# Kernel optimization log

Hardware: AMD Instinct MI355X
Metric: run time of the kernel (lower is better)

The kernel has to match this reference:

```python
import jax, jax.numpy as jnp
import numpy as np

N_STATE = 1024
N_HEAD = 16
LENGTHS = np.array([512, 576, 640, 704, 768, 832, 896, 1024], dtype=np.int32)
BATCH = len(LENGTHS)
MAX_SEQLEN = int(LENGTHS.max())
N_CTX = int(LENGTHS.sum())


def setup_inputs() -> dict:
    key = jax.random.key(0)
    ks = jax.random.split(key, 8)
    d = N_STATE
    cu = np.concatenate([[0], np.cumsum(LENGTHS)]).astype(np.int32)
    return {
        "x": jax.random.normal(ks[0], (N_CTX, d), dtype=jnp.float32),
        "Wq": jax.random.normal(ks[1], (d, d), dtype=jnp.float32) * 0.02,
        "bq": jnp.zeros((d,), dtype=jnp.float32),
        "Wk": jax.random.normal(ks[2], (d, d), dtype=jnp.float32) * 0.02,
        "Wv": jax.random.normal(ks[3], (d, d), dtype=jnp.float32) * 0.02,
        "bv": jnp.zeros((d,), dtype=jnp.float32),
        "Wo": jax.random.normal(ks[4], (d, d), dtype=jnp.float32) * 0.02,
        "bo": jnp.zeros((d,), dtype=jnp.float32),
        "cu_seqlens": jnp.asarray(cu),
    }


def reference(x, Wq, bq, Wk, Wv, bv, Wo, bo, cu_seqlens):
    n_ctx, d = x.shape
    H, hd = N_HEAD, d // N_HEAD
    scale = hd ** -0.5
    B, S = BATCH, MAX_SEQLEN  # static pad shape

    # QKV projections (torch Linear convention: y = x @ W.T + b; key has no bias)
    q = (x @ Wq.T + bq).reshape(n_ctx, H, hd)
    k = (x @ Wk.T).reshape(n_ctx, H, hd)
    v = (x @ Wv.T + bv).reshape(n_ctx, H, hd)

    seqlens = cu_seqlens[1:] - cu_seqlens[:-1]          # [B]
    tok = jnp.arange(n_ctx)
    seg = jnp.searchsorted(cu_seqlens[1:], tok, side="right")  # [n_ctx] batch id
    pos = tok - cu_seqlens[seg]                          # [n_ctx] position in seq

    # scatter packed tokens into zero-padded [B, S, H, hd]
    qp = jnp.zeros((B, S, H, hd), q.dtype).at[seg, pos].set(q)
    kp = jnp.zeros((B, S, H, hd), k.dtype).at[seg, pos].set(k)
    vp = jnp.zeros((B, S, H, hd), v.dtype).at[seg, pos].set(v)

    valid = jnp.arange(S)[None, :] < seqlens[:, None]    # [B, S] key mask

    scores = jnp.einsum("bihd,bjhd->bhij", qp, kp) * scale   # [B, H, S, S]
    neg = -jnp.finfo(scores.dtype).max
    scores = jnp.where(valid[:, None, None, :], scores, neg)
    weights = jax.nn.softmax(scores, axis=-1)
    ctx = jnp.einsum("bhij,bjhd->bihd", weights, vp)         # [B, S, H, hd]

    # gather back to packed [n_ctx, d]
    packed = ctx[seg, pos].reshape(n_ctx, d)
    return packed @ Wo.T + bo
```

## Files before the change

### kernel.cpp

```cpp
#include <hip/hip_runtime.h>
#include <hip/hip_fp16.h>
#include <stdint.h>

#define NCTX 5952
#define NHEAD 16
#define NABLK 372
#define NWBLK 256

typedef _Float16 f16x8 __attribute__((ext_vector_type(8)));
typedef _Float16 f16x4 __attribute__((ext_vector_type(4)));
typedef float    f32x4 __attribute__((ext_vector_type(4)));

typedef const __attribute__((address_space(1))) void* gp1;
typedef __attribute__((address_space(3))) void* lp3;

__device__ __forceinline__ f32x4 mfma16(f16x8 a, f16x8 b, f32x4 c) {
    return __builtin_amdgcn_mfma_f32_16x16x32_f16(a, b, c, 0, 0, 0);
}

#define SBAR() do { __builtin_amdgcn_sched_barrier(0); \
                    __builtin_amdgcn_s_barrier();      \
                    __builtin_amdgcn_sched_barrier(0); } while (0)

__device__ const int kQT[9]    = {0, 4, 9, 14, 20, 26, 33, 40, 48};
__device__ const int kBASE8[8] = {0, 512, 1088, 1728, 2432, 3200, 4032, 4928};
__device__ const int kLEN[8]   = {512, 576, 640, 704, 768, 832, 896, 1024};


__global__ __launch_bounds__(256) void presplit_all(
    const float* __restrict__ x,
    const float* __restrict__ Wq, const float* __restrict__ Wk,
    const float* __restrict__ Wv, const float* __restrict__ Wo,
    _Float16* __restrict__ Ah, _Float16* __restrict__ Wh)
{
    constexpr int NAG = NABLK * 32 * 64;
    const int idx = blockIdx.x * 256 + threadIdx.x;
    const float* src;
    _Float16* dst;
    if (idx < NAG) {
        int chunk = idx >> 6, within = idx & 63;
        int t = chunk & 31, b = chunk >> 5;
        int rb = within >> 2, go = within & 3;
        int r = b * 16 + rb;
        int g = go ^ ((r >> 1) & 3);
        src = x + (size_t)r * 1024 + t * 32 + g * 8;
        dst = Ah + (size_t)idx * 8;
    } else {
        int i2 = idx - NAG;
        int chunk = i2 >> 6, within = i2 & 63;
        int t = chunk & 31, b = chunk >> 5;
        int rb = within >> 2, go = within & 3;
        int n = b * 16 + rb;
        int g = go ^ ((n >> 1) & 3);
        const float* s = (n < 1024) ? Wq : (n < 2048) ? Wk : (n < 3072) ? Wv : Wo;
        src = s + (size_t)(n & 1023) * 1024 + t * 32 + g * 8;
        dst = Wh + (size_t)i2 * 8;
    }
    f32x4 v0 = *(const f32x4*)src;
    f32x4 v1 = *(const f32x4*)(src + 4);
    f16x8 hv;
    #pragma unroll
    for (int e = 0; e < 4; ++e) { hv[e] = (_Float16)v0[e]; hv[4 + e] = (_Float16)v1[e]; }
    *(f16x8*)dst = hv;
}

template <int MODE>
__global__ __launch_bounds__(512) void gemm1p(
    const _Float16* __restrict__ Ag, const _Float16* __restrict__ Wg,
    const float* __restrict__ bq, const float* __restrict__ bv, const float* __restrict__ bo,
    _Float16* __restrict__ qh, _Float16* __restrict__ kh, _Float16* __restrict__ vt,
    float* __restrict__ outp)
{
    constexpr int BN   = (MODE == 0) ? 384 : 128;
    constexpr int MI   = 6;
    constexpr int NF   = BN / 64;
    constexpr int SPH  = (MODE == 0) ? 5 : 3;
    constexpr int SPL  = (MODE == 0) ? 4 : 2;
    constexpr int ABYT = 12288;
    constexpr int BBYT = BN * 64;
    constexpr int BUF  = ABYT + BBYT;
    constexpr int T    = 32;
    constexpr int WB0  = (MODE == 0) ? 0 : 192;

    __shared__ __align__(16) char lds[3 * BUF];

    int bid = blockIdx.x;
    bid = (bid & 7) * 31 + (bid >> 3);
    const int mt = bid % 31, nt = bid / 31;
    const int m0 = mt * 192, n0 = nt * BN;
    const int tid = threadIdx.x;
    const int w = tid >> 6, l = tid & 63;
    const int ls = l >> 4, lq = l & 15;
    const int wm = w >> 2, wn = w & 3;

    const int myspw = (w < 4) ? SPH : SPL;
    const int fbase = (w < 4) ? w * SPH : 4 * SPH + (w - 4) * SPL;

    const char* sbase[5];
    int ldst[5];
    #pragma unroll
    for (int s = 0; s < 5; ++s) {
        if (s < myspw) {
            int f = fbase + s;
            if (f < 12) sbase[s] = (const char*)Ag + ((size_t)(m0 / 16 + f) * 32) * 1024;
            else        sbase[s] = (const char*)Wg + ((size_t)(WB0 + n0 / 16 + (f - 12)) * 32) * 1024;
            ldst[s] = f * 1024;
        } else { sbase[s] = nullptr; ldst[s] = 0; }
    }
    const int l16 = l * 16;
    auto STG = [&](int buf, int t2) {
        #pragma unroll
        for (int s = 0; s < 5; ++s)
            if (s < myspw)
                __builtin_amdgcn_global_load_lds((gp1)(sbase[s] + (size_t)t2 * 1024 + l16),
                                                 (lp3)(lds + buf * BUF + ldst[s]), 16, 0, 0);
    };

    int aoA[MI], aoB[NF];
    #pragma unroll
    for (int i = 0; i < MI; ++i) {
        int r = wm * 96 + i * 16 + lq;
        aoA[i] = r * 64 + 16 * (ls ^ ((r >> 1) & 3));
    }
    #pragma unroll
    for (int j = 0; j < NF; ++j) {
        int r = wn * (16 * NF) + j * 16 + lq;
        aoB[j] = ABYT + r * 64 + 16 * (ls ^ ((r >> 1) & 3));
    }

    f32x4 acc[MI][NF] = {};

    STG(0, 0);
    STG(1, 1);
    if (w < 4) { if constexpr (SPH == 5) asm volatile("s_waitcnt vmcnt(5)" ::: "memory");
                 else                    asm volatile("s_waitcnt vmcnt(3)" ::: "memory"); }
    else       { if constexpr (SPL == 4) asm volatile("s_waitcnt vmcnt(4)" ::: "memory");
                 else                    asm volatile("s_waitcnt vmcnt(2)" ::: "memory"); }
    SBAR();

    int cb = 0, pb = 2;
    #pragma unroll 1
    for (int t = 0; t < T; ++t) {
        const bool pf = (t + 2 < T);
        const char* cbp = lds + cb * BUF;
        if (pf) STG(pb, t + 2);

        f16x8 ah[MI], b[NF];
        #pragma unroll
        for (int i = 0; i < MI; ++i) ah[i] = *(const f16x8*)(cbp + aoA[i]);
        #pragma unroll
        for (int j = 0; j < NF; ++j) b[j] = *(const f16x8*)(cbp + aoB[j]);
        __builtin_amdgcn_s_setprio(1);
        #pragma unroll
        for (int i = 0; i < MI; ++i)
            #pragma unroll
            for (int j = 0; j < NF; ++j)
                acc[i][j] = mfma16(ah[i], b[j], acc[i][j]);
        __builtin_amdgcn_s_setprio(0);

        if (pf) {
            if (w < 4) { if constexpr (SPH == 5) asm volatile("s_waitcnt vmcnt(5) lgkmcnt(0)" ::: "memory");
                         else                    asm volatile("s_waitcnt vmcnt(3) lgkmcnt(0)" ::: "memory"); }
            else       { if constexpr (SPL == 4) asm volatile("s_waitcnt vmcnt(4) lgkmcnt(0)" ::: "memory");
                         else                    asm volatile("s_waitcnt vmcnt(2) lgkmcnt(0)" ::: "memory"); }
        } else {
            asm volatile("s_waitcnt vmcnt(0) lgkmcnt(0)" ::: "memory");
        }
        SBAR();
        cb = (cb == 2) ? 0 : cb + 1;
        pb = (pb == 2) ? 0 : pb + 1;
    }

    #pragma unroll
    for (int i = 0; i < MI; ++i)
        #pragma unroll
        for (int j = 0; j < NF; ++j) {
            const int mb = m0 + wm * 96 + i * 16 + 4 * ls;
            const int n  = n0 + wn * (16 * NF) + j * 16 + lq;
            if (MODE == 0) {
                const int which = n >> 10, nn = n & 1023;
                const int hh = nn >> 6, dd = nn & 63;
                if (which == 2) {
                    f16x4 vv;
                    #pragma unroll
                    for (int r = 0; r < 4; ++r) vv[r] = (_Float16)(acc[i][j][r] + bv[nn]);
                    *(f16x4*)&vt[((size_t)hh * 64 + dd) * NCTX + mb] = vv;
                } else if (which == 0) {
                    #pragma unroll
                    for (int r = 0; r < 4; ++r)
                        qh[((size_t)hh * NCTX + mb + r) * 64 + dd] = (_Float16)(acc[i][j][r] + bq[nn]);
                } else {
                    #pragma unroll
                    for (int r = 0; r < 4; ++r)
                        kh[((size_t)hh * NCTX + mb + r) * 64 + dd] = (_Float16)acc[i][j][r];
                }
            } else {
                #pragma unroll
                for (int r = 0; r < 4; ++r)
                    outp[(size_t)(mb + r) * 1024 + n] = acc[i][j][r] + bo[n];
            }
        }
}

__global__ __launch_bounds__(256) void attn_kernel(
    const _Float16* __restrict__ qh, const _Float16* __restrict__ kh,
    const _Float16* __restrict__ vt,
    _Float16* __restrict__ Ahc)
{
    __shared__ alignas(16) _Float16 KT[2][64][64];
    __shared__ alignas(16) _Float16 VT[2][64][64];
    __shared__ alignas(16) _Float16 P[4][2][16][64];
    const int bid = blockIdx.x;
    const int hd = bid & 15, t = bid >> 4;
    int b = 0;
    while (t >= kQT[b + 1]) ++b;
    const int kbase = kBASE8[b];
    const int L = kLEN[b];
    const int w = threadIdx.x >> 6, l = threadIdx.x & 63;
    const int ls = l >> 4, lq = l & 15;
    const int xm = lq & 7;
    const int q0l = (t - kQT[b]) * 128 + w * 32;
    const bool active = (q0l < L);
    const int q0 = kbase + q0l;

    const _Float16* kb = kh + (size_t)hd * NCTX * 64;
    const _Float16* vb = vt + (size_t)hd * 64 * NCTX;

    const char* ksrc[2]; const char* vsrc[2]; int sdst[2];
    #pragma unroll
    for (int s = 0; s < 2; ++s) {
        int G = w * 128 + s * 64 + l;
        int row = G >> 3, g = G & 7;
        ksrc[s] = (const char*)(kb + ((size_t)(kbase + row)) * 64 + (size_t)((g ^ (row & 7)) * 8));
        vsrc[s] = (const char*)(vb + (size_t)row * NCTX + kbase + (size_t)((g ^ (row & 7)) * 8));
        sdst[s] = (w * 128 + s * 64) * 16;
    }
    auto STG = [&](int buf, int t2) {
        #pragma unroll
        for (int s = 0; s < 2; ++s)
            __builtin_amdgcn_global_load_lds((gp1)(ksrc[s] + (size_t)t2 * 8192),
                                             (lp3)((char*)&KT[buf][0][0] + sdst[s]), 16, 0, 0);
        #pragma unroll
        for (int s = 0; s < 2; ++s)
            __builtin_amdgcn_global_load_lds((gp1)(vsrc[s] + (size_t)t2 * 128),
                                             (lp3)((char*)&VT[buf][0][0] + sdst[s]), 16, 0, 0);
    };

    f16x8 qf[2][2];
    if (active) {
        #pragma unroll
        for (int qg = 0; qg < 2; ++qg) {
            const _Float16* qp = qh + ((size_t)hd * NCTX + q0 + qg * 16 + lq) * 64 + ls * 8;
            qf[qg][0] = *(const f16x8*)qp;
            qf[qg][1] = *(const f16x8*)(qp + 32);
        }
    }

    f32x4 acc[2][4] = {};
    float lsum[2] = {0.f, 0.f};
    const int nst = L >> 6;

    STG(0, 0);
    #pragma unroll 1
    for (int tt = 0; tt < nst; ++tt) {
        const int buf = tt & 1;
        if (tt + 1 < nst) {
            STG(buf ^ 1, tt + 1);
            asm volatile("s_waitcnt vmcnt(4)" ::: "memory");
        } else {
            asm volatile("s_waitcnt vmcnt(0)" ::: "memory");
        }
        SBAR();

        if (active) {
            f32x4 s[2][4];
            __builtin_amdgcn_s_setprio(1);
            #pragma unroll
            for (int g = 0; g < 4; ++g) {
                const char* kp = (const char*)&KT[buf][g * 16 + lq][0];
                f16x8 kf0 = *(const f16x8*)(kp + ((ls ^ xm) * 16));
                f16x8 kf1 = *(const f16x8*)(kp + (((ls + 4) ^ xm) * 16));
                #pragma unroll
                for (int qg = 0; qg < 2; ++qg) {
                    f32x4 z = {};
                    z = mfma16(kf0, qf[qg][0], z);
                    z = mfma16(kf1, qf[qg][1], z);
                    s[qg][g] = z;
                }
            }
            __builtin_amdgcn_s_setprio(0);
            #pragma unroll
            for (int qg = 0; qg < 2; ++qg) {
                float tsum = 0.f;
                #pragma unroll
                for (int g = 0; g < 4; ++g) {
                    f16x4 ph;
                    #pragma unroll
                    for (int r = 0; r < 4; ++r) {
                        float pv = __expf(s[qg][g][r] * 0.125f);
                        tsum += pv;
                        ph[r] = (_Float16)pv;
                    }
                    int gi = 2 * g + (ls >> 1);
                    *(f16x4*)&P[w][qg][lq][(((gi ^ (lq & 7)) << 3) | ((ls & 1) << 2))] = ph;
                }
                tsum += __shfl_xor(tsum, 16, 64);
                tsum += __shfl_xor(tsum, 32, 64);
                lsum[qg] += tsum;
            }
            __builtin_amdgcn_s_setprio(1);
            #pragma unroll
            for (int c = 0; c < 2; ++c) {
                f16x8 pf[2];
                #pragma unroll
                for (int qg = 0; qg < 2; ++qg)
                    pf[qg] = *(const f16x8*)&P[w][qg][lq][((4 * c + ls) ^ (lq & 7)) << 3];
                #pragma unroll
                for (int dg = 0; dg < 4; ++dg) {
                    const char* vp = (const char*)&VT[buf][dg * 16 + lq][0];
                    f16x8 vf = *(const f16x8*)(vp + (((c * 4 + ls) ^ xm) * 16));
                    #pragma unroll
                    for (int qg = 0; qg < 2; ++qg)
                        acc[qg][dg] = mfma16(vf, pf[qg], acc[qg][dg]);
                }
            }
            __builtin_amdgcn_s_setprio(0);
        }

        asm volatile("s_waitcnt lgkmcnt(0)" ::: "memory");
        SBAR();
    }

    if (active) {
        #pragma unroll
        for (int qg = 0; qg < 2; ++qg) {
            const float inv = 1.f / lsum[qg];
            const int m = q0 + qg * 16 + lq;
            const int bA = m >> 4, rbA = m & 15, xr = (m >> 1) & 3;
            #pragma unroll
            for (int dg = 0; dg < 4; ++dg) {
                const int k  = hd * 64 + dg * 16 + 4 * ls;
                const int tK = k >> 5;
                const int gs = ((k >> 3) & 3) ^ xr;
                const int e  = k & 7;
                f16x4 ch;
                #pragma unroll
                for (int r = 0; r < 4; ++r) ch[r] = (_Float16)(acc[qg][dg][r] * inv);
                *(f16x4*)((char*)Ahc + ((size_t)(bA * 32 + tK)) * 1024 + rbA * 64 + gs * 16 + e * 2) = ch;
            }
        }
    }
}

extern "C" void kernel_launch(void* const* d_in, const int* in_sizes, int n_in,
                              void* d_out, int out_size, void* d_ws, size_t ws_size,
                              hipStream_t stream)
{
    const float* x  = (const float*)d_in[0];
    const float* Wq = (const float*)d_in[1];
    const float* bq = (const float*)d_in[2];
    const float* Wk = (const float*)d_in[3];
    const float* Wv = (const float*)d_in[4];
    const float* bv = (const float*)d_in[5];
    const float* Wo = (const float*)d_in[6];
    const float* bo = (const float*)d_in[7];
    float* out = (float*)d_out;

    char* p = (char*)d_ws;
    _Float16* Ah  = (_Float16*)p; p += (size_t)NCTX * 1024 * 2;
    _Float16* Wh  = (_Float16*)p; p += (size_t)4096 * 1024 * 2;
    _Float16* qh  = (_Float16*)p; p += (size_t)NHEAD * NCTX * 64 * 2;
    _Float16* kh  = (_Float16*)p; p += (size_t)NHEAD * NCTX * 64 * 2;
    _Float16* vt  = (_Float16*)p; p += (size_t)NHEAD * NCTX * 64 * 2;
    _Float16* Ahc = (_Float16*)p; p += (size_t)NCTX * 1024 * 2;

    presplit_all<<<dim3((NABLK * 32 * 64 + NWBLK * 32 * 64) / 256), 256, 0, stream>>>(
        x, Wq, Wk, Wv, Wo, Ah, Wh);
    gemm1p<0><<<dim3(248), 512, 0, stream>>>(Ah, Wh, bq, bv, nullptr,
                                             qh, kh, vt, nullptr);
    attn_kernel<<<dim3(48 * 16), 256, 0, stream>>>(qh, kh, vt, Ahc);
    gemm1p<1><<<dim3(248), 512, 0, stream>>>(Ahc, Wh, nullptr, nullptr, bo,
                                             nullptr, nullptr, nullptr, out);
}
```

Baseline: 126.9 us.

## Double K-tile to 64 and switch GEMM staging from triple to double buffering

```diff
diff --git a/kernel.cpp b/kernel.cpp
--- a/kernel.cpp
+++ b/kernel.cpp
@@ -74,15 +74,14 @@
     constexpr int BN   = (MODE == 0) ? 384 : 128;
     constexpr int MI   = 6;
     constexpr int NF   = BN / 64;
-    constexpr int SPH  = (MODE == 0) ? 5 : 3;
-    constexpr int SPL  = (MODE == 0) ? 4 : 2;
-    constexpr int ABYT = 12288;
-    constexpr int BBYT = BN * 64;
-    constexpr int BUF  = ABYT + BBYT;
-    constexpr int T    = 32;
+    constexpr int TOT  = 24 + 2 * (BN / 16);
+    constexpr int SPW  = TOT / 8;
+    constexpr int ABP  = 24 * 1024;
+    constexpr int BUF  = ABP + (BN / 16) * 2048;
+    constexpr int T    = 16;
     constexpr int WB0  = (MODE == 0) ? 0 : 192;
 
-    __shared__ __align__(16) char lds[3 * BUF];
+    __shared__ __align__(16) char lds[2 * BUF];
 
     int bid = blockIdx.x;
     bid = (bid & 7) * 31 + (bid >> 3);
@@ -93,82 +92,69 @@
     const int ls = l >> 4, lq = l & 15;
     const int wm = w >> 2, wn = w & 3;
 
-    const int myspw = (w < 4) ? SPH : SPL;
-    const int fbase = (w < 4) ? w * SPH : 4 * SPH + (w - 4) * SPL;
-
-    const char* sbase[5];
-    int ldst[5];
-    #pragma unroll
-    for (int s = 0; s < 5; ++s) {
-        if (s < myspw) {
-            int f = fbase + s;
-            if (f < 12) sbase[s] = (const char*)Ag + ((size_t)(m0 / 16 + f) * 32) * 1024;
-            else        sbase[s] = (const char*)Wg + ((size_t)(WB0 + n0 / 16 + (f - 12)) * 32) * 1024;
-            ldst[s] = f * 1024;
-        } else { sbase[s] = nullptr; ldst[s] = 0; }
+    const char* sbase[SPW];
+    int ldst[SPW];
+    #pragma unroll
+    for (int s = 0; s < SPW; ++s) {
+        int c = w * SPW + s;
+        if (c < 24) {
+            int f = c >> 1, sub = c & 1;
+            sbase[s] = (const char*)Ag + (size_t)(m0 / 16 + f) * 32768 + sub * 1024;
+        } else {
+            int cB = c - 24, f = cB >> 1, sub = cB & 1;
+            sbase[s] = (const char*)Wg + (size_t)(WB0 + n0 / 16 + f) * 32768 + sub * 1024;
+        }
+        ldst[s] = c * 1024;
     }
     const int l16 = l * 16;
     auto STG = [&](int buf, int t2) {
         #pragma unroll
-        for (int s = 0; s < 5; ++s)
-            if (s < myspw)
-                __builtin_amdgcn_global_load_lds((gp1)(sbase[s] + (size_t)t2 * 1024 + l16),
-                                                 (lp3)(lds + buf * BUF + ldst[s]), 16, 0, 0);
+        for (int s = 0; s < SPW; ++s)
+            __builtin_amdgcn_global_load_lds((gp1)(sbase[s] + (size_t)t2 * 2048 + l16),
+                                             (lp3)(lds + buf * BUF + ldst[s]), 16, 0, 0);
     };
 
     int aoA[MI], aoB[NF];
     #pragma unroll
     for (int i = 0; i < MI; ++i) {
         int r = wm * 96 + i * 16 + lq;
-        aoA[i] = r * 64 + 16 * (ls ^ ((r >> 1) & 3));
+        aoA[i] = (r >> 4) * 2048 + (r & 15) * 64 + ((ls ^ ((r >> 1) & 3)) << 4);
     }
     #pragma unroll
     for (int j = 0; j < NF; ++j) {
         int r = wn * (16 * NF) + j * 16 + lq;
-        aoB[j] = ABYT + r * 64 + 16 * (ls ^ ((r >> 1) & 3));
+        aoB[j] = ABP + (r >> 4) * 2048 + (r & 15) * 64 + ((ls ^ ((r >> 1) & 3)) << 4);
     }
 
     f32x4 acc[MI][NF] = {};
 
     STG(0, 0);
-    STG(1, 1);
-    if (w < 4) { if constexpr (SPH == 5) asm volatile("s_waitcnt vmcnt(5)" ::: "memory");
-                 else                    asm volatile("s_waitcnt vmcnt(3)" ::: "memory"); }
-    else       { if constexpr (SPL == 4) asm volatile("s_waitcnt vmcnt(4)" ::: "memory");
-                 else                    asm volatile("s_waitcnt vmcnt(2)" ::: "memory"); }
+    asm volatile("s_waitcnt vmcnt(0)" ::: "memory");
     SBAR();
 
-    int cb = 0, pb = 2;
     #pragma unroll 1
     for (int t = 0; t < T; ++t) {
-        const bool pf = (t + 2 < T);
-        const char* cbp = lds + cb * BUF;
-        if (pf) STG(pb, t + 2);
-
-        f16x8 ah[MI], b[NF];
-        #pragma unroll
-        for (int i = 0; i < MI; ++i) ah[i] = *(const f16x8*)(cbp + aoA[i]);
-        #pragma unroll
-        for (int j = 0; j < NF; ++j) b[j] = *(const f16x8*)(cbp + aoB[j]);
-        __builtin_amdgcn_s_setprio(1);
-        #pragma unroll
-        for (int i = 0; i < MI; ++i)
-            #pragma unroll
-            for (int j = 0; j < NF; ++j)
-                acc[i][j] = mfma16(ah[i], b[j], acc[i][j]);
-        __builtin_amdgcn_s_setprio(0);
-
-        if (pf) {
-            if (w < 4) { if constexpr (SPH == 5) asm volatile("s_waitcnt vmcnt(5) lgkmcnt(0)" ::: "memory");
-                         else                    asm volatile("s_waitcnt vmcnt(3) lgkmcnt(0)" ::: "memory"); }
-            else       { if constexpr (SPL == 4) asm volatile("s_waitcnt vmcnt(4) lgkmcnt(0)" ::: "memory");
-                         else                    asm volatile("s_waitcnt vmcnt(2) lgkmcnt(0)" ::: "memory"); }
-        } else {
-            asm volatile("s_waitcnt vmcnt(0) lgkmcnt(0)" ::: "memory");
-        }
+        const char* cbp = lds + (t & 1) * BUF;
+        if (t + 1 < T) STG((t + 1) & 1, t + 1);
+
+        #pragma unroll
+        for (int kc = 0; kc < 2; ++kc) {
+            f16x8 ah[MI], b[NF];
+            #pragma unroll
+            for (int i = 0; i < MI; ++i) ah[i] = *(const f16x8*)(cbp + aoA[i] + kc * 1024);
+            #pragma unroll
+            for (int j = 0; j < NF; ++j) b[j] = *(const f16x8*)(cbp + aoB[j] + kc * 1024);
+            __builtin_amdgcn_s_setprio(1);
+            #pragma unroll
+            for (int i = 0; i < MI; ++i)
+                #pragma unroll
+                for (int j = 0; j < NF; ++j)
+                    acc[i][j] = mfma16(ah[i], b[j], acc[i][j]);
+            __builtin_amdgcn_s_setprio(0);
+        }
+
+        asm volatile("s_waitcnt vmcnt(0) lgkmcnt(0)" ::: "memory");
         SBAR();
-        cb = (cb == 2) ? 0 : cb + 1;
-        pb = (pb == 2) ? 0 : pb + 1;
     }
 
     #pragma unroll
```

After: 126.5 us, median of 3. No clear change (-0.3%).
